# Kernel tuning notes

Measured on AMD Instinct MI355X. Metric: run time of the kernel, lower is better.

The kernel has to match this reference:

```python
import jax, jax.numpy as jnp
import numpy as np

BETA = 0.95
THR = 1.0  # snntorch Leaky default threshold

# Heaviside spike with ATan surrogate gradient (snntorch default, alpha=2):
# d/dx = 1 / (1 + (pi*x)^2)
@jax.custom_vjp
def spike_fn(x):
    return (x > 0).astype(x.dtype)

def _spike_fwd(x):
    return spike_fn(x), x

def _spike_bwd(x, g):
    return (g / (1.0 + (jnp.pi * x) ** 2),)

spike_fn.defvjp(_spike_fwd, _spike_bwd)


def setup_inputs() -> dict:
    key = jax.random.key(0)
    ks = jax.random.split(key, 5)
    T, B, D_in, D_h, D_out = 25, 4096, 784, 1000, 10
    x = jax.random.normal(ks[0], (T, B, D_in), dtype=jnp.float32)
    # Kaiming-uniform-ish init like nn.Linear
    w1 = jax.random.uniform(ks[1], (D_h, D_in), jnp.float32, -1, 1) / np.sqrt(D_in)
    b1 = jax.random.uniform(ks[2], (D_h,), jnp.float32, -1, 1) / np.sqrt(D_in)
    w2 = jax.random.uniform(ks[3], (D_out, D_h), jnp.float32, -1, 1) / np.sqrt(D_h)
    b2 = jax.random.uniform(ks[4], (D_out,), jnp.float32, -1, 1) / np.sqrt(D_h)
    return {"x": x, "w1": w1, "b1": b1, "w2": w2, "b2": b2}


def reference(x, w1, b1, w2, b2):
    B = x.shape[1]
    mem1_0 = jnp.zeros((B, w1.shape[0]), x.dtype)
    mem2_0 = jnp.zeros((B, w2.shape[0]), x.dtype)

    def step(carry, xt):
        mem1, mem2 = carry
        # layer 1: Linear + Leaky (reset-by-subtraction, reset from prior mem)
        cur1 = xt @ w1.T + b1
        reset1 = spike_fn(mem1 - THR)
        mem1 = BETA * mem1 + cur1 - reset1 * THR
        spk1 = spike_fn(mem1 - THR)
        # layer 2
        cur2 = spk1 @ w2.T + b2
        reset2 = spike_fn(mem2 - THR)
        mem2 = BETA * mem2 + cur2 - reset2 * THR
        spk2 = spike_fn(mem2 - THR)
        return (mem1, mem2), spk2

    (mem1, mem2), spk_rec = jax.lax.scan(step, (mem1_0, mem2_0), x)
    return spk_rec, mem2
```

## Files before the change

### kernel.cpp

```cpp
#include <hip/hip_runtime.h>

typedef _Float16 f16;
typedef _Float16 f16x4 __attribute__((ext_vector_type(4)));
typedef _Float16 f16x8 __attribute__((ext_vector_type(8)));
typedef float f32x4 __attribute__((ext_vector_type(4)));

#define T_STEPS 25
#define BATCH   4096
#define DIN     784
#define DH      1000
#define HP      1024
#define DOUT    10
#define MROWS   (T_STEPS * BATCH)
#define KSEG    800
#define KA      (2 * KSEG)
#define KB      (3 * KSEG)
#define BM      128
#define BN      128
#define BK      32

#define GLOAD_LDS16(gptr, lptr) \
    __builtin_amdgcn_global_load_lds( \
        (const __attribute__((address_space(1))) void*)(gptr), \
        (__attribute__((address_space(3))) void*)(lptr), 16, 0, 0)

__global__ void aconv_kernel(const float* __restrict__ x, f16* __restrict__ Ah)
{
    const int total = MROWS * 200;
    for (int idx = blockIdx.x * blockDim.x + threadIdx.x; idx < total;
         idx += gridDim.x * blockDim.x) {
        const int r  = idx / 200;
        const int c4 = (idx - r * 200) * 4;
        f16x4 hi, lo;
        if (c4 < DIN) {
            const float4 v = *(const float4*)(x + (size_t)r * DIN + c4);
            const float vv[4] = {v.x, v.y, v.z, v.w};
            #pragma unroll
            for (int j = 0; j < 4; ++j) {
                f16 h = (f16)vv[j];
                hi[j] = h;
                lo[j] = (f16)(vv[j] - (float)h);
            }
        } else {
            #pragma unroll
            for (int j = 0; j < 4; ++j) { hi[j] = (f16)0.f; lo[j] = (f16)0.f; }
        }
        *(f16x4*)(Ah + (size_t)r * KA + c4)        = hi;
        *(f16x4*)(Ah + (size_t)r * KA + KSEG + c4) = lo;
    }
}

__global__ void wconv_kernel(const float* __restrict__ w1, const float* __restrict__ b1,
                             const float* __restrict__ w2,
                             f16* __restrict__ Wh, float* __restrict__ b1p,
                             float* __restrict__ w2t)
{
    const int stride = gridDim.x * blockDim.x;
    const int tid0 = blockIdx.x * blockDim.x + threadIdx.x;
    for (int idx = tid0; idx < HP * KB; idx += stride) {
        const int n  = idx / KB;
        const int k  = idx - n * KB;
        const int seg = k / KSEG;
        const int kc  = k - seg * KSEG;
        float w = (n < DH && kc < DIN) ? w1[n * DIN + kc] : 0.f;
        f16 h = (f16)w;
        Wh[idx] = (seg < 2) ? h : (f16)(w - (float)h);
    }
    for (int idx = tid0; idx < HP; idx += stride)
        b1p[idx] = (idx < DH) ? b1[idx] : 0.f;
    for (int idx = tid0; idx < HP * DOUT; idx += stride) {
        const int h = idx / DOUT;
        const int o = idx - h * DOUT;
        w2t[idx] = (h < DH) ? w2[o * DH + h] : 0.f;
    }
}

__global__ __launch_bounds__(256, 2)
void gemm_kernel(const f16* __restrict__ A, const f16* __restrict__ B,
                 const float* __restrict__ bias, float* __restrict__ C)
{
    __shared__ f16 As[BM * BK];
    __shared__ f16 Bs[BN * BK];

    const int bid = blockIdx.x;
    const int swz = (bid & 7) * 800 + (bid >> 3);
    const int mt = swz >> 3;
    const int nt = swz & 7;
    const int rowBase = mt * BM;
    const int colBase = nt * BN;

    const int tid  = threadIdx.x;
    const int wave = tid >> 6;
    const int lane = tid & 63;
    const int wm = wave >> 1, wn = wave & 1;

    const int srow = tid >> 2;
    const int scol = (tid & 3) * 8;
    const f16* Ag0 = A + (size_t)(rowBase + srow) * KA + scol;
    const f16* Ag1 = Ag0 + (size_t)64 * KA;
    const f16* Bg0 = B + (size_t)(colBase + srow) * KB + scol;
    const f16* Bg1 = Bg0 + (size_t)64 * KB;
    f16* Al0 = As + (wave * 16) * BK;
    f16* Al1 = As + (64 + wave * 16) * BK;
    f16* Bl0 = Bs + (wave * 16) * BK;
    f16* Bl1 = Bs + (64 + wave * 16) * BK;

    f32x4 acc[4][4];
    #pragma unroll
    for (int m = 0; m < 4; ++m)
        #pragma unroll
        for (int n = 0; n < 4; ++n)
            acc[m][n] = (f32x4){0.f, 0.f, 0.f, 0.f};

    const int arow = wm * 64 + (lane & 15);
    const int brow = wn * 64 + (lane & 15);
    const int kg   = (lane >> 4) * 8;

    for (int kk = 0; kk < KB; kk += BK) {
        const int ak = (kk < KA) ? kk : (kk - KA);
        GLOAD_LDS16(Ag0 + ak, Al0);
        GLOAD_LDS16(Ag1 + ak, Al1);
        GLOAD_LDS16(Bg0 + kk, Bl0);
        GLOAD_LDS16(Bg1 + kk, Bl1);
        __syncthreads();

        f16x8 af[4], bf[4];
        #pragma unroll
        for (int m = 0; m < 4; ++m)
            af[m] = *(const f16x8*)&As[(arow + m * 16) * BK + kg];
        #pragma unroll
        for (int n = 0; n < 4; ++n)
            bf[n] = *(const f16x8*)&Bs[(brow + n * 16) * BK + kg];
        #pragma unroll
        for (int m = 0; m < 4; ++m)
            #pragma unroll
            for (int n = 0; n < 4; ++n)
                acc[m][n] = __builtin_amdgcn_mfma_f32_16x16x32_f16(
                    af[m], bf[n], acc[m][n], 0, 0, 0);
        __syncthreads();
    }

    const int c_col0 = colBase + wn * 64 + (lane & 15);
    const int c_row0 = rowBase + wm * 64 + (lane >> 4) * 4;
    #pragma unroll
    for (int n = 0; n < 4; ++n) {
        const int gcol = c_col0 + n * 16;
        const float bv = bias[gcol];
        #pragma unroll
        for (int m = 0; m < 4; ++m) {
            const int grow = c_row0 + m * 16;
            #pragma unroll
            for (int r = 0; r < 4; ++r)
                C[(size_t)(grow + r) * HP + gcol] = acc[m][n][r] + bv;
        }
    }
}

__global__ __launch_bounds__(256)
void phase2_kernel(const float* __restrict__ cur1, const float* __restrict__ w2t,
                   const float* __restrict__ b2, float* __restrict__ out)
{
    __shared__ float w2s[HP * DOUT];
    const int tid = threadIdx.x;
    for (int i = tid; i < HP * DOUT; i += 256) w2s[i] = w2t[i];

    const int lane = tid & 63;
    const int wave = tid >> 6;
    const int b = blockIdx.x * 4 + wave;

    float m1[16];
    #pragma unroll
    for (int i = 0; i < 16; ++i) m1[i] = 0.f;
    float m2[DOUT], b2r[DOUT];
    #pragma unroll
    for (int o = 0; o < DOUT; ++o) { m2[o] = 0.f; b2r[o] = b2[o]; }
    __syncthreads();

    for (int t = 0; t < T_STEPS; ++t) {
        const float* cr = cur1 + ((size_t)t * BATCH + b) * HP;
        float p[DOUT];
        #pragma unroll
        for (int o = 0; o < DOUT; ++o) p[o] = 0.f;

        #pragma unroll
        for (int c = 0; c < 4; ++c) {
            const float4 cu = *(const float4*)(cr + c * 256 + lane * 4);
            const float cv[4] = {cu.x, cu.y, cu.z, cu.w};
            #pragma unroll
            for (int j = 0; j < 4; ++j) {
                const float mo = m1[c * 4 + j];
                const float rs = (mo > 1.0f) ? 1.0f : 0.0f;
                const float mn = 0.95f * mo + cv[j] - rs;
                m1[c * 4 + j] = mn;
                if (mn > 1.0f) {
                    const float* wr = w2s + (c * 256 + lane * 4 + j) * DOUT;
                    #pragma unroll
                    for (int o = 0; o < DOUT; ++o) p[o] += wr[o];
                }
            }
        }
        #pragma unroll
        for (int o = 0; o < DOUT; ++o) {
            float v = p[o];
            #pragma unroll
            for (int msk = 32; msk > 0; msk >>= 1) v += __shfl_xor(v, msk, 64);
            p[o] = v;
        }
        #pragma unroll
        for (int o = 0; o < DOUT; ++o) {
            const float cur2 = p[o] + b2r[o];
            const float mo = m2[o];
            const float rs = (mo > 1.0f) ? 1.0f : 0.0f;
            m2[o] = 0.95f * mo + cur2 - rs;
        }
        if (lane < DOUT)
            out[(size_t)t * (BATCH * DOUT) + (size_t)b * DOUT + lane] =
                (m2[lane] > 1.0f) ? 1.0f : 0.0f;
    }
    if (lane < DOUT)
        out[(size_t)T_STEPS * BATCH * DOUT + (size_t)b * DOUT + lane] = m2[lane];
}

extern "C" void kernel_launch(void* const* d_in, const int* in_sizes, int n_in,
                              void* d_out, int out_size, void* d_ws, size_t ws_size,
                              hipStream_t stream)
{
    const float* x  = (const float*)d_in[0];
    const float* w1 = (const float*)d_in[1];
    const float* b1 = (const float*)d_in[2];
    const float* w2 = (const float*)d_in[3];
    const float* b2 = (const float*)d_in[4];
    float* out = (float*)d_out;

    char* wsb = (char*)d_ws;
    f16*   Ah   = (f16*)(wsb);
    f16*   Wh   = (f16*)(wsb + 327680000);
    float* cur1 = (float*)(wsb + 327680000 + 4915200);
    float* b1p  = (float*)(wsb + 327680000 + 4915200 + 419430400);
    float* w2t  = (float*)(wsb + 327680000 + 4915200 + 419430400 + 4096);

    aconv_kernel<<<4096, 256, 0, stream>>>(x, Ah);
    wconv_kernel<<<1024, 256, 0, stream>>>(w1, b1, w2, Wh, b1p, w2t);
    gemm_kernel<<<6400, 256, 0, stream>>>(Ah, Wh, b1p, cur1);
    phase2_kernel<<<1024, 256, 0, stream>>>(cur1, w2t, b2, out);
}
```

Measured before the change: 887.0 us.

## Rewrite GEMM with 256x256 tiles, 4-stage LDS pipeline and swizzled layout

The GEMM kernel moves from 128x128 tiles with single-buffered LDS and two syncthreads per k-step to 256x256 tiles on 512-thread blocks. It adds a 4-stage global-to-LDS prefetch ring with explicit vmcnt waits, split barriers, and raised priority around the MFMA bursts. An XOR swizzle on the LDS column groups is meant to avoid bank conflicts. The larger tiles improve data reuse and the deeper pipeline hides load latency, at the cost of 128KB of LDS and more accumulator registers per block, which may limit occupancy.

```diff
diff --git a/kernel.cpp b/kernel.cpp
--- a/kernel.cpp
+++ b/kernel.cpp
@@ -15,14 +15,7 @@
 #define KSEG    800
 #define KA      (2 * KSEG)
 #define KB      (3 * KSEG)
-#define BM      128
-#define BN      128
-#define BK      32
-
-#define GLOAD_LDS16(gptr, lptr) \
-    __builtin_amdgcn_global_load_lds( \
-        (const __attribute__((address_space(1))) void*)(gptr), \
-        (__attribute__((address_space(3))) void*)(lptr), 16, 0, 0)
+#define NTILES  (KB / 32)
 
 __global__ void aconv_kernel(const float* __restrict__ x, f16* __restrict__ Ah)
 {
@@ -75,83 +68,135 @@
     }
 }
 
-__global__ __launch_bounds__(256, 2)
+#define GL(gp, ldsoff) __builtin_amdgcn_global_load_lds( \
+    (const __attribute__((address_space(1))) void*)(gp), \
+    (__attribute__((address_space(3))) void*)(lds + (ldsoff)), 16, 0, 0)
+
+#define STAGE_A(tt) do { \
+    const int ak_ = (((tt) < 50) ? (tt) : ((tt) - 50)) * 32; \
+    GL(Ag + ak_,            ((tt) & 3) * 8192 + widoff); \
+    GL(Ag + ak_ + 128 * KA, ((tt) & 3) * 8192 + 4096 + widoff); } while (0)
+#define STAGE_B(tt) do { \
+    const int bk_ = (tt) * 32; \
+    GL(Bg + bk_,                     32768 + ((tt) & 3) * 8192 + widoff); \
+    GL(Bg + bk_ + (size_t)128 * KB,  32768 + ((tt) & 3) * 8192 + 4096 + widoff); } while (0)
+
+#define MFMA16(M0) \
+    acc[M0+0][0] = __builtin_amdgcn_mfma_f32_16x16x32_f16(af0, bf0, acc[M0+0][0], 0, 0, 0); \
+    acc[M0+0][1] = __builtin_amdgcn_mfma_f32_16x16x32_f16(af0, bf1, acc[M0+0][1], 0, 0, 0); \
+    acc[M0+0][2] = __builtin_amdgcn_mfma_f32_16x16x32_f16(af0, bf2, acc[M0+0][2], 0, 0, 0); \
+    acc[M0+0][3] = __builtin_amdgcn_mfma_f32_16x16x32_f16(af0, bf3, acc[M0+0][3], 0, 0, 0); \
+    acc[M0+1][0] = __builtin_amdgcn_mfma_f32_16x16x32_f16(af1, bf0, acc[M0+1][0], 0, 0, 0); \
+    acc[M0+1][1] = __builtin_amdgcn_mfma_f32_16x16x32_f16(af1, bf1, acc[M0+1][1], 0, 0, 0); \
+    acc[M0+1][2] = __builtin_amdgcn_mfma_f32_16x16x32_f16(af1, bf2, acc[M0+1][2], 0, 0, 0); \
+    acc[M0+1][3] = __builtin_amdgcn_mfma_f32_16x16x32_f16(af1, bf3, acc[M0+1][3], 0, 0, 0); \
+    acc[M0+2][0] = __builtin_amdgcn_mfma_f32_16x16x32_f16(af2, bf0, acc[M0+2][0], 0, 0, 0); \
+    acc[M0+2][1] = __builtin_amdgcn_mfma_f32_16x16x32_f16(af2, bf1, acc[M0+2][1], 0, 0, 0); \
+    acc[M0+2][2] = __builtin_amdgcn_mfma_f32_16x16x32_f16(af2, bf2, acc[M0+2][2], 0, 0, 0); \
+    acc[M0+2][3] = __builtin_amdgcn_mfma_f32_16x16x32_f16(af2, bf3, acc[M0+2][3], 0, 0, 0); \
+    acc[M0+3][0] = __builtin_amdgcn_mfma_f32_16x16x32_f16(af3, bf0, acc[M0+3][0], 0, 0, 0); \
+    acc[M0+3][1] = __builtin_amdgcn_mfma_f32_16x16x32_f16(af3, bf1, acc[M0+3][1], 0, 0, 0); \
+    acc[M0+3][2] = __builtin_amdgcn_mfma_f32_16x16x32_f16(af3, bf2, acc[M0+3][2], 0, 0, 0); \
+    acc[M0+3][3] = __builtin_amdgcn_mfma_f32_16x16x32_f16(af3, bf3, acc[M0+3][3], 0, 0, 0);
+
+#define BODY(tt, STG, WAITSTR) do { \
+    const int bA = ((tt) & 3) * 8192; \
+    const int bB = 32768 + ((tt) & 3) * 8192; \
+    f16x8 af0, af1, af2, af3, bf0, bf1, bf2, bf3; \
+     \
+    af0 = *(const f16x8*)(lds + bA + aoffb + 0 * 512); \
+    af1 = *(const f16x8*)(lds + bA + aoffb + 1 * 512); \
+    af2 = *(const f16x8*)(lds + bA + aoffb + 2 * 512); \
+    af3 = *(const f16x8*)(lds + bA + aoffb + 3 * 512); \
+    bf0 = *(const f16x8*)(lds + bB + boffb + 0 * 512); \
+    bf1 = *(const f16x8*)(lds + bB + boffb + 1 * 512); \
+    bf2 = *(const f16x8*)(lds + bB + boffb + 2 * 512); \
+    bf3 = *(const f16x8*)(lds + bB + boffb + 3 * 512); \
+    if (STG) STAGE_A((tt) + 3); \
+    __builtin_amdgcn_s_barrier(); \
+    asm volatile("s_waitcnt lgkmcnt(0)" ::: "memory"); \
+    __builtin_amdgcn_sched_barrier(0); \
+    __builtin_amdgcn_s_setprio(1); \
+    MFMA16(0) \
+    __builtin_amdgcn_s_setprio(0); \
+    __builtin_amdgcn_s_barrier(); \
+     \
+    af0 = *(const f16x8*)(lds + bA + aoffb + 4 * 512); \
+    af1 = *(const f16x8*)(lds + bA + aoffb + 5 * 512); \
+    af2 = *(const f16x8*)(lds + bA + aoffb + 6 * 512); \
+    af3 = *(const f16x8*)(lds + bA + aoffb + 7 * 512); \
+    if (STG) STAGE_B((tt) + 3); \
+    asm volatile(WAITSTR ::: "memory"); \
+    __builtin_amdgcn_s_barrier(); \
+    asm volatile("s_waitcnt lgkmcnt(0)" ::: "memory"); \
+    __builtin_amdgcn_sched_barrier(0); \
+    __builtin_amdgcn_s_setprio(1); \
+    MFMA16(4) \
+    __builtin_amdgcn_s_setprio(0); \
+    __builtin_amdgcn_s_barrier(); \
+} while (0)
+
+__global__ __launch_bounds__(512, 2)
 void gemm_kernel(const f16* __restrict__ A, const f16* __restrict__ B,
                  const float* __restrict__ bias, float* __restrict__ C)
 {
-    __shared__ f16 As[BM * BK];
-    __shared__ f16 Bs[BN * BK];
+    __shared__ f16 lds[65536];
 
     const int bid = blockIdx.x;
-    const int swz = (bid & 7) * 800 + (bid >> 3);
-    const int mt = swz >> 3;
-    const int nt = swz & 7;
-    const int rowBase = mt * BM;
-    const int colBase = nt * BN;
+    const int swz = (bid & 7) * 200 + (bid >> 3);
+    const int mt = swz >> 2;
+    const int nt = swz & 3;
+    const size_t rowBase = (size_t)mt * 256;
+    const int colBase = nt * 256;
 
     const int tid  = threadIdx.x;
-    const int wave = tid >> 6;
+    const int wid  = tid >> 6;
     const int lane = tid & 63;
-    const int wm = wave >> 1, wn = wave & 1;
+    const int wm = wid >> 2;
+    const int wn = wid & 3;
 
     const int srow = tid >> 2;
-    const int scol = (tid & 3) * 8;
-    const f16* Ag0 = A + (size_t)(rowBase + srow) * KA + scol;
-    const f16* Ag1 = Ag0 + (size_t)64 * KA;
-    const f16* Bg0 = B + (size_t)(colBase + srow) * KB + scol;
-    const f16* Bg1 = Bg0 + (size_t)64 * KB;
-    f16* Al0 = As + (wave * 16) * BK;
-    f16* Al1 = As + (64 + wave * 16) * BK;
-    f16* Bl0 = Bs + (wave * 16) * BK;
-    f16* Bl1 = Bs + (64 + wave * 16) * BK;
-
-    f32x4 acc[4][4];
-    #pragma unroll
-    for (int m = 0; m < 4; ++m)
+    const int g = (tid & 3) ^ ((tid >> 3) & 3);
+    const f16* Ag = A + (rowBase + srow) * KA + g * 8;
+    const f16* Bg = B + (size_t)(colBase + srow) * KB + g * 8;
+    const int widoff = wid * 512;
+
+    const int cq = (lane >> 4) ^ (((lane & 15) >> 1) & 3);
+    const int aoffb = (wm * 128 + (lane & 15)) * 32 + cq * 8;
+    const int boffb = (wn * 64  + (lane & 15)) * 32 + cq * 8;
+
+    f32x4 acc[8][4];
+    #pragma unroll
+    for (int m = 0; m < 8; ++m)
         #pragma unroll
         for (int n = 0; n < 4; ++n)
             acc[m][n] = (f32x4){0.f, 0.f, 0.f, 0.f};
 
-    const int arow = wm * 64 + (lane & 15);
-    const int brow = wn * 64 + (lane & 15);
-    const int kg   = (lane >> 4) * 8;
-
-    for (int kk = 0; kk < KB; kk += BK) {
-        const int ak = (kk < KA) ? kk : (kk - KA);
-        GLOAD_LDS16(Ag0 + ak, Al0);
-        GLOAD_LDS16(Ag1 + ak, Al1);
-        GLOAD_LDS16(Bg0 + kk, Bl0);
-        GLOAD_LDS16(Bg1 + kk, Bl1);
-        __syncthreads();
-
-        f16x8 af[4], bf[4];
-        #pragma unroll
-        for (int m = 0; m < 4; ++m)
-            af[m] = *(const f16x8*)&As[(arow + m * 16) * BK + kg];
-        #pragma unroll
-        for (int n = 0; n < 4; ++n)
-            bf[n] = *(const f16x8*)&Bs[(brow + n * 16) * BK + kg];
-        #pragma unroll
-        for (int m = 0; m < 4; ++m)
-            #pragma unroll
-            for (int n = 0; n < 4; ++n)
-                acc[m][n] = __builtin_amdgcn_mfma_f32_16x16x32_f16(
-                    af[m], bf[n], acc[m][n], 0, 0, 0);
-        __syncthreads();
-    }
+    STAGE_A(0 - 3 + 3); STAGE_B(0);
+    STAGE_A(1);         STAGE_B(1);
+    STAGE_A(2);         STAGE_B(2);
+    asm volatile("s_waitcnt vmcnt(8)" ::: "memory");
+    __builtin_amdgcn_s_barrier();
+
+    #pragma unroll 4
+    for (int t = 0; t < NTILES - 3; ++t)
+        BODY(t, 1, "s_waitcnt vmcnt(8)");
+    BODY(NTILES - 3, 0, "s_waitcnt vmcnt(4)");
+    BODY(NTILES - 2, 0, "s_waitcnt vmcnt(0)");
+    BODY(NTILES - 1, 0, "");
 
     const int c_col0 = colBase + wn * 64 + (lane & 15);
-    const int c_row0 = rowBase + wm * 64 + (lane >> 4) * 4;
+    const size_t c_row0 = rowBase + wm * 128 + (lane >> 4) * 4;
     #pragma unroll
     for (int n = 0; n < 4; ++n) {
         const int gcol = c_col0 + n * 16;
         const float bv = bias[gcol];
         #pragma unroll
-        for (int m = 0; m < 4; ++m) {
-            const int grow = c_row0 + m * 16;
+        for (int m = 0; m < 8; ++m) {
+            const size_t grow = c_row0 + m * 16;
             #pragma unroll
             for (int r = 0; r < 4; ++r)
-                C[(size_t)(grow + r) * HP + gcol] = acc[m][n][r] + bv;
+                C[(grow + r) * HP + gcol] = acc[m][n][r] + bv;
         }
     }
 }
@@ -241,6 +286,6 @@
 
     aconv_kernel<<<4096, 256, 0, stream>>>(x, Ah);
     wconv_kernel<<<1024, 256, 0, stream>>>(w1, b1, w2, Wh, b1p, w2t);
-    gemm_kernel<<<6400, 256, 0, stream>>>(Ah, Wh, b1p, cur1);
+    gemm_kernel<<<1600, 512, 0, stream>>>(Ah, Wh, b1p, cur1);
     phase2_kernel<<<1024, 256, 0, stream>>>(cur1, w2t, b2, out);
 }
```

Result: faster. 764.2 us (-13.9%).
